# Optimization experiments

Measured on AMD Instinct MI355X. Metric: run time of the kernel, lower is better.

The kernel has to match this reference:

```python
import math
import jax, jax.numpy as jnp
import numpy as np

B, S, D, H = 64, 577, 768, 12
DH = D // H          # 64 per-head dim
FF = 4 * D           # 3072 intermediate
EPS = 1e-6


def layernorm(x, g, b):
    mu = jnp.mean(x, axis=-1, keepdims=True)
    var = jnp.mean(jnp.square(x - mu), axis=-1, keepdims=True)
    return (x - mu) * jax.lax.rsqrt(var + EPS) * g + b


def gelu_tanh(x):
    # NewGELUActivation: 0.5*x*(1+tanh(sqrt(2/pi)*(x+0.044715*x^3)))
    c = math.sqrt(2.0 / math.pi)
    return 0.5 * x * (1.0 + jnp.tanh(c * (x + 0.044715 * x ** 3)))


def setup_inputs() -> dict:
    key = jax.random.key(0)
    ks = jax.random.split(key, 16)
    s_d = 1.0 / math.sqrt(D)
    s_ff = 1.0 / math.sqrt(FF)
    return {
        "x": jax.random.normal(ks[0], (B, S, D), jnp.float32),
        "ln1_g": jnp.ones((D,), jnp.float32),
        "ln1_b": jnp.zeros((D,), jnp.float32),
        # per-head Q/K/V weights stacked: [H, D, DH] (equivalent to H separate Linears)
        "Wq": jax.random.normal(ks[1], (H, D, DH), jnp.float32) * s_d,
        "bq": jax.random.normal(ks[2], (H, DH), jnp.float32) * 0.01,
        "Wk": jax.random.normal(ks[3], (H, D, DH), jnp.float32) * s_d,
        "bk": jax.random.normal(ks[4], (H, DH), jnp.float32) * 0.01,
        "Wv": jax.random.normal(ks[5], (H, D, DH), jnp.float32) * s_d,
        "bv": jax.random.normal(ks[6], (H, DH), jnp.float32) * 0.01,
        "Wo": jax.random.normal(ks[7], (D, D), jnp.float32) * s_d,
        "bo": jax.random.normal(ks[8], (D,), jnp.float32) * 0.01,
        "ln2_g": jnp.ones((D,), jnp.float32),
        "ln2_b": jnp.zeros((D,), jnp.float32),
        "W1": jax.random.normal(ks[9], (D, FF), jnp.float32) * s_d,
        "b1": jax.random.normal(ks[10], (FF,), jnp.float32) * 0.01,
        "W2": jax.random.normal(ks[11], (FF, D), jnp.float32) * s_ff,
        "b2": jax.random.normal(ks[12], (D,), jnp.float32) * 0.01,
    }


def reference(x, ln1_g, ln1_b, Wq, bq, Wk, bk, Wv, bv, Wo, bo,
              ln2_g, ln2_b, W1, b1, W2, b2):
    # --- pre-norm MHA ---
    h = layernorm(x, ln1_g, ln1_b)                       # [B,S,D]
    q = jnp.einsum('bsd,hde->bhse', h, Wq) + bq[:, None, :]
    k = jnp.einsum('bsd,hde->bhse', h, Wk) + bk[:, None, :]
    v = jnp.einsum('bsd,hde->bhse', h, Wv) + bv[:, None, :]
    scores = jnp.einsum('bhse,bhte->bhst', q, k) / math.sqrt(DH)
    probs = jax.nn.softmax(scores, axis=-1)              # [B,H,S,S]
    attn = jnp.einsum('bhst,bhte->bhse', probs, v)       # [B,H,S,DH]
    # concat heads in head order -> [B,S,H*DH]
    concat = attn.transpose(0, 2, 1, 3).reshape(B, S, H * DH)
    x = x + concat @ Wo + bo
    # --- pre-norm MLP ---
    m = layernorm(x, ln2_g, ln2_b)
    m = gelu_tanh(m @ W1 + b1) @ W2 + b2
    return x + m
```

## Files before the change

### kernel.cpp

```cpp
#include <hip/hip_runtime.h>
#include <stdint.h>

constexpr int BZ   = 64;
constexpr int SEQ  = 577;
constexpr int DM   = 768;
constexpr int NH   = 12;
constexpr int HD   = 64;
constexpr int FFD  = 3072;
constexpr int ROWS = BZ * SEQ;
constexpr int BHN  = BZ * NH;
constexpr int VTS  = 640;

typedef __attribute__((ext_vector_type(8))) short bf16x8;
typedef __attribute__((ext_vector_type(4))) float f32x4;

static __device__ __forceinline__ unsigned short f2bf(float f) {
  union { float f; uint32_t u; } v; v.f = f;
  uint32_t r = (v.u + 0x7FFFu + ((v.u >> 16) & 1u)) >> 16;
  return (unsigned short)r;
}

static __device__ __forceinline__ f32x4 mfma16(bf16x8 a, bf16x8 b, f32x4 c) {
  return __builtin_amdgcn_mfma_f32_16x16x32_bf16(a, b, c, 0, 0, 0);
}

static __device__ __forceinline__ void gload_lds16(const unsigned short* g, unsigned short* l) {
  __builtin_amdgcn_global_load_lds((const __attribute__((address_space(1))) unsigned int*)g,
                                   (__attribute__((address_space(3))) unsigned int*)l, 16, 0, 0);
}

__global__ __launch_bounds__(256) void prep_qkv(const float* __restrict__ Wq,
                                                const float* __restrict__ Wk,
                                                const float* __restrict__ Wv,
                                                unsigned short* __restrict__ dst) {
  int tid = blockIdx.x * 256 + threadIdx.x;
  int n = tid / DM, k = tid - n * DM;
  int seg = n / DM;
  int within = n - seg * DM;
  int h = within >> 6, e = within & 63;
  const float* W = (seg == 0) ? Wq : (seg == 1) ? Wk : Wv;
  dst[tid] = f2bf(W[((size_t)h * DM + k) * HD + e]);
}

__global__ __launch_bounds__(256) void prep_t(const float* __restrict__ src,
                                              unsigned short* __restrict__ dst,
                                              int N, int K) {
  int tid = blockIdx.x * 256 + threadIdx.x;
  if (tid >= N * K) return;
  int n = tid / K, k = tid - n * K;
  dst[tid] = f2bf(src[(size_t)k * N + n]);
}

__global__ __launch_bounds__(256) void ln_bf16(const float* __restrict__ X,
                                               const float* __restrict__ g,
                                               const float* __restrict__ b,
                                               unsigned short* __restrict__ out) {
  int row  = blockIdx.x * 4 + (threadIdx.x >> 6);
  int lane = threadIdx.x & 63;
  const float* x = X + (size_t)row * DM;
  float4 v[3];
  float s = 0.f, s2 = 0.f;
#pragma unroll
  for (int i = 0; i < 3; i++) {
    v[i] = *(const float4*)(x + i * 256 + lane * 4);
    s  += v[i].x + v[i].y + v[i].z + v[i].w;
    s2 += v[i].x * v[i].x + v[i].y * v[i].y + v[i].z * v[i].z + v[i].w * v[i].w;
  }
#pragma unroll
  for (int o = 1; o < 64; o <<= 1) { s += __shfl_xor(s, o); s2 += __shfl_xor(s2, o); }
  float mu  = s * (1.f / DM);
  float var = s2 * (1.f / DM) - mu * mu;
  float inv = rsqrtf(var + 1e-6f);
#pragma unroll
  for (int i = 0; i < 3; i++) {
    int c = i * 256 + lane * 4;
    float4 gg = *(const float4*)(g + c);
    float4 bb = *(const float4*)(b + c);
    ushort4 o4;
    o4.x = f2bf((v[i].x - mu) * inv * gg.x + bb.x);
    o4.y = f2bf((v[i].y - mu) * inv * gg.y + bb.y);
    o4.z = f2bf((v[i].z - mu) * inv * gg.z + bb.z);
    o4.w = f2bf((v[i].w - mu) * inv * gg.w + bb.w);
    *(ushort4*)(out + (size_t)row * DM + c) = o4;
  }
}

template <int EPI>
__global__ __launch_bounds__(256) void gemm_bt(
    const unsigned short* __restrict__ A, const unsigned short* __restrict__ Bt,
    int M, int N, int K,
    const float* __restrict__ bias0, const float* __restrict__ bias1,
    const float* __restrict__ bias2, const float* __restrict__ xres,
    float* __restrict__ outf,
    unsigned short* __restrict__ ob0, unsigned short* __restrict__ ob1,
    unsigned short* __restrict__ ob2) {
  __shared__ __align__(16) unsigned short sA[128 * 32];
  __shared__ __align__(16) unsigned short sB[128 * 32];
  const int tid  = threadIdx.x;
  const int wave = tid >> 6, lane = tid & 63;
  const int l15 = lane & 15, quad = lane >> 4;
  const int m0 = blockIdx.y * 128, n0 = blockIdx.x * 128;
  const int wm = (wave >> 1) * 64, wn = (wave & 1) * 64;

  f32x4 acc[4][4] = {};
  const int nkt = K >> 5;
  for (int kt = 0; kt < nkt; ++kt) {
#pragma unroll
    for (int i = 0; i < 2; i++) {
      int c = tid + i * 256;
      int row = c >> 2, kc = (c & 3) << 3;
      int ra = m0 + row; if (ra >= M) ra = M - 1;
      gload_lds16(A  + (size_t)ra * K         + (kt << 5) + kc, sA + row * 32 + kc);
      gload_lds16(Bt + (size_t)(n0 + row) * K + (kt << 5) + kc, sB + row * 32 + kc);
    }
    __syncthreads();
    bf16x8 aF[4], bF[4];
#pragma unroll
    for (int mi = 0; mi < 4; mi++) aF[mi] = *(const bf16x8*)(sA + (wm + mi * 16 + l15) * 32 + quad * 8);
#pragma unroll
    for (int ni = 0; ni < 4; ni++) bF[ni] = *(const bf16x8*)(sB + (wn + ni * 16 + l15) * 32 + quad * 8);
#pragma unroll
    for (int mi = 0; mi < 4; mi++)
#pragma unroll
      for (int ni = 0; ni < 4; ni++) acc[mi][ni] = mfma16(aF[mi], bF[ni], acc[mi][ni]);
    __syncthreads();
  }

#pragma unroll
  for (int mi = 0; mi < 4; mi++) {
#pragma unroll
    for (int r = 0; r < 4; r++) {
      int mg = m0 + wm + mi * 16 + quad * 4 + r;
      if (mg >= M) continue;
      if constexpr (EPI == 0) {
        int bb = mg / SEQ, ss = mg - bb * SEQ;
        int seg = n0 / DM;
        int within0 = n0 - seg * DM + wn;
#pragma unroll
        for (int ni = 0; ni < 4; ni++) {
          int wcol = within0 + ni * 16 + l15;
          int h = wcol >> 6, e = wcol & 63;
          float val = acc[mi][ni][r];
          if (seg == 0) {
            float qv = (val + bias0[wcol]) * 0.125f;
            ob0[((size_t)(bb * NH + h) * SEQ + ss) * HD + e] = f2bf(qv);
          } else if (seg == 1) {
            float kv = val + bias1[wcol];
            ob1[((size_t)(bb * NH + h) * SEQ + ss) * HD + e] = f2bf(kv);
          } else {
            float vv = val + bias2[wcol];
            ob2[((size_t)(bb * NH + h) * HD + e) * VTS + ss] = f2bf(vv);
          }
        }
      } else if constexpr (EPI == 1) {
        size_t base = (size_t)mg * DM;
#pragma unroll
        for (int ni = 0; ni < 4; ni++) {
          int col = n0 + wn + ni * 16 + l15;
          outf[base + col] = xres[base + col] + acc[mi][ni][r] + bias0[col];
        }
      } else if constexpr (EPI == 2) {
        size_t base = (size_t)mg * FFD;
#pragma unroll
        for (int ni = 0; ni < 4; ni++) {
          int col = n0 + wn + ni * 16 + l15;
          float xv = acc[mi][ni][r] + bias0[col];
          float u  = 0.7978845608028654f * (xv + 0.044715f * xv * xv * xv);
          float uc = fminf(fmaxf(u, -15.f), 15.f);
          float t  = __expf(2.f * uc);
          float gel = 0.5f * xv * (1.f + (t - 1.f) / (t + 1.f));
          ob0[base + col] = f2bf(gel);
        }
      } else {
        size_t base = (size_t)mg * DM;
#pragma unroll
        for (int ni = 0; ni < 4; ni++) {
          int col = n0 + wn + ni * 16 + l15;
          outf[base + col] += acc[mi][ni][r] + bias0[col];
        }
      }
    }
  }
}

__global__ __launch_bounds__(256) void attn_fused(
    const unsigned short* __restrict__ Q, const unsigned short* __restrict__ Kb,
    const unsigned short* __restrict__ Vt, unsigned short* __restrict__ Cc) {
  __shared__ __align__(16) unsigned short sK[64 * 72];
  __shared__ __align__(16) unsigned short sV[64 * 72];
  __shared__ __align__(16) unsigned short sP[4][16 * 72];
  const int tid  = threadIdx.x;
  const int wave = tid >> 6, lane = tid & 63;
  const int quad = lane >> 4, l15 = lane & 15;
  const int bh = blockIdx.y;
  const int q0 = blockIdx.x * 64;

  int qr = q0 + wave * 16 + l15; if (qr > SEQ - 1) qr = SEQ - 1;
  const unsigned short* qrow = Q + ((size_t)bh * SEQ + qr) * HD;
  bf16x8 aQ0 = *(const bf16x8*)(qrow + quad * 8);
  bf16x8 aQ1 = *(const bf16x8*)(qrow + 32 + quad * 8);

  float m[4], l[4];
  f32x4 accO[4] = {};
#pragma unroll
  for (int r = 0; r < 4; r++) { m[r] = -3e38f; l[r] = 0.f; }

  for (int t0 = 0; t0 < SEQ; t0 += 64) {
#pragma unroll
    for (int i = 0; i < 2; i++) {
      int c = tid + i * 256;
      int row = c >> 3, col = (c & 7) << 3;
      int tk = t0 + row; if (tk > SEQ - 1) tk = SEQ - 1;
      bf16x8 vk = *(const bf16x8*)(Kb + ((size_t)bh * SEQ + tk) * HD + col);
      bf16x8 vv = *(const bf16x8*)(Vt + ((size_t)bh * HD + row) * VTS + t0 + col);
      *(bf16x8*)(sK + row * 72 + col) = vk;
      *(bf16x8*)(sV + row * 72 + col) = vv;
    }
    __syncthreads();

    f32x4 s4[4];
#pragma unroll
    for (int ni = 0; ni < 4; ni++) {
      bf16x8 b0 = *(const bf16x8*)(sK + (ni * 16 + l15) * 72 + quad * 8);
      bf16x8 b1 = *(const bf16x8*)(sK + (ni * 16 + l15) * 72 + 32 + quad * 8);
      f32x4 a = {0.f, 0.f, 0.f, 0.f};
      a = mfma16(aQ0, b0, a);
      a = mfma16(aQ1, b1, a);
      s4[ni] = a;
    }
#pragma unroll
    for (int ni = 0; ni < 4; ni++) {
      if (t0 + ni * 16 + l15 >= SEQ) {
#pragma unroll
        for (int r = 0; r < 4; r++) s4[ni][r] = -3e38f;
      }
    }
    float mn[4], alpha[4], ts[4];
#pragma unroll
    for (int r = 0; r < 4; r++) {
      float tm = fmaxf(fmaxf(s4[0][r], s4[1][r]), fmaxf(s4[2][r], s4[3][r]));
#pragma unroll
      for (int o = 1; o < 16; o <<= 1) tm = fmaxf(tm, __shfl_xor(tm, o));
      mn[r] = fmaxf(m[r], tm);
      alpha[r] = __expf(m[r] - mn[r]);
      m[r] = mn[r];
      ts[r] = 0.f;
    }
#pragma unroll
    for (int ni = 0; ni < 4; ni++) {
#pragma unroll
      for (int r = 0; r < 4; r++) {
        float p = __expf(s4[ni][r] - mn[r]);
        ts[r] += p;
        sP[wave][(quad * 4 + r) * 72 + ni * 16 + l15] = f2bf(p);
      }
    }
#pragma unroll
    for (int r = 0; r < 4; r++) {
#pragma unroll
      for (int o = 1; o < 16; o <<= 1) ts[r] += __shfl_xor(ts[r], o);
      l[r] = l[r] * alpha[r] + ts[r];
#pragma unroll
      for (int ni = 0; ni < 4; ni++) accO[ni][r] *= alpha[r];
    }
    bf16x8 aP0 = *(const bf16x8*)(sP[wave] + l15 * 72 + quad * 8);
    bf16x8 aP1 = *(const bf16x8*)(sP[wave] + l15 * 72 + 32 + quad * 8);
#pragma unroll
    for (int ni = 0; ni < 4; ni++) {
      bf16x8 v0 = *(const bf16x8*)(sV + (ni * 16 + l15) * 72 + quad * 8);
      bf16x8 v1 = *(const bf16x8*)(sV + (ni * 16 + l15) * 72 + 32 + quad * 8);
      accO[ni] = mfma16(aP0, v0, accO[ni]);
      accO[ni] = mfma16(aP1, v1, accO[ni]);
    }
    __syncthreads();
  }

  int bb = bh / NH, h = bh - bb * NH;
#pragma unroll
  for (int r = 0; r < 4; r++) {
    int ss = q0 + wave * 16 + quad * 4 + r;
    if (ss < SEQ) {
      float inv = 1.f / l[r];
      size_t base = ((size_t)bb * SEQ + ss) * DM + h * HD;
#pragma unroll
      for (int ni = 0; ni < 4; ni++)
        Cc[base + ni * 16 + l15] = f2bf(accO[ni][r] * inv);
    }
  }
}

extern "C" void kernel_launch(void* const* d_in, const int* in_sizes, int n_in,
                              void* d_out, int out_size, void* d_ws, size_t ws_size,
                              hipStream_t stream) {
  (void)in_sizes; (void)n_in; (void)out_size; (void)ws_size;
  const float* x     = (const float*)d_in[0];
  const float* ln1_g = (const float*)d_in[1];
  const float* ln1_b = (const float*)d_in[2];
  const float* Wq    = (const float*)d_in[3];
  const float* bq    = (const float*)d_in[4];
  const float* Wk    = (const float*)d_in[5];
  const float* bk    = (const float*)d_in[6];
  const float* Wv    = (const float*)d_in[7];
  const float* bv    = (const float*)d_in[8];
  const float* Wo    = (const float*)d_in[9];
  const float* bo    = (const float*)d_in[10];
  const float* ln2_g = (const float*)d_in[11];
  const float* ln2_b = (const float*)d_in[12];
  const float* W1    = (const float*)d_in[13];
  const float* b1    = (const float*)d_in[14];
  const float* W2    = (const float*)d_in[15];
  const float* b2    = (const float*)d_in[16];
  float* out = (float*)d_out;

  char* ws = (char*)d_ws;
  size_t off = 0;
  auto alloc = [&](size_t bytes) -> unsigned short* {
    unsigned short* p = (unsigned short*)(ws + off);
    off += (bytes + 255) & ~(size_t)255;
    return p;
  };
  unsigned short* h_bf  = alloc((size_t)ROWS * DM * 2);
  unsigned short* q_bf  = alloc((size_t)BHN * SEQ * HD * 2);
  unsigned short* k_bf  = alloc((size_t)BHN * SEQ * HD * 2);
  unsigned short* vt_bf = alloc((size_t)BHN * HD * VTS * 2);
  unsigned short* cc_bf = alloc((size_t)ROWS * DM * 2);
  unsigned short* g_bf = q_bf;
  unsigned short* wqkv_t = alloc((size_t)2304 * 768 * 2);
  unsigned short* w1_t   = alloc((size_t)3072 * 768 * 2);
  unsigned short* w2_t   = alloc((size_t)768 * 3072 * 2);
  unsigned short* wo_t   = alloc((size_t)768 * 768 * 2);

  prep_qkv<<<(2304 * 768) / 256, 256, 0, stream>>>(Wq, Wk, Wv, wqkv_t);
  prep_t<<<(3072 * 768) / 256, 256, 0, stream>>>(W1, w1_t, 3072, 768);
  prep_t<<<(768 * 3072) / 256, 256, 0, stream>>>(W2, w2_t, 768, 3072);
  prep_t<<<(768 * 768) / 256, 256, 0, stream>>>(Wo, wo_t, 768, 768);

  ln_bf16<<<ROWS / 4, 256, 0, stream>>>(x, ln1_g, ln1_b, h_bf);
  gemm_bt<0><<<dim3(2304 / 128, (ROWS + 127) / 128), 256, 0, stream>>>(
      h_bf, wqkv_t, ROWS, 2304, 768, bq, bk, bv, nullptr, nullptr, q_bf, k_bf, vt_bf);
  attn_fused<<<dim3((SEQ + 63) / 64, BHN), 256, 0, stream>>>(q_bf, k_bf, vt_bf, cc_bf);
  gemm_bt<1><<<dim3(768 / 128, (ROWS + 127) / 128), 256, 0, stream>>>(
      cc_bf, wo_t, ROWS, 768, 768, bo, nullptr, nullptr, x, out, nullptr, nullptr, nullptr);
  ln_bf16<<<ROWS / 4, 256, 0, stream>>>(out, ln2_g, ln2_b, h_bf);
  gemm_bt<2><<<dim3(3072 / 128, (ROWS + 127) / 128), 256, 0, stream>>>(
      h_bf, w1_t, ROWS, 3072, 768, b1, nullptr, nullptr, nullptr, nullptr, g_bf, nullptr, nullptr);
  gemm_bt<3><<<dim3(768 / 128, (ROWS + 127) / 128), 256, 0, stream>>>(
      g_bf, w2_t, ROWS, 768, 3072, b2, nullptr, nullptr, nullptr, out, nullptr, nullptr, nullptr);
}
```

Baseline: 1.599 ms.

## Use 64-wide K tiles with XOR-swizzled LDS and XCD-aware block remap in GEMMs

The GEMM K step goes from 32 to 64, which halves the number of barrier pairs per tile and doubles the MFMA work done between syncs. LDS rows are XOR-swizzled so fragment reads avoid bank conflicts on the wider rows. A 1D grid is remapped so consecutive tiles land on the same XCD (chunks of 8), aiming to improve L2 reuse of A and B tiles. The cost is twice the LDS per block, which may reduce occupancy.

```diff
diff --git a/kernel.cpp b/kernel.cpp
--- a/kernel.cpp
+++ b/kernel.cpp
@@ -88,41 +88,54 @@
 template <int EPI>
 __global__ __launch_bounds__(256) void gemm_bt(
     const unsigned short* __restrict__ A, const unsigned short* __restrict__ Bt,
-    int M, int N, int K,
+    int M, int N, int K, int nbn,
     const float* __restrict__ bias0, const float* __restrict__ bias1,
     const float* __restrict__ bias2, const float* __restrict__ xres,
     float* __restrict__ outf,
     unsigned short* __restrict__ ob0, unsigned short* __restrict__ ob1,
     unsigned short* __restrict__ ob2) {
-  __shared__ __align__(16) unsigned short sA[128 * 32];
-  __shared__ __align__(16) unsigned short sB[128 * 32];
+  __shared__ __align__(16) unsigned short sA[128 * 64];
+  __shared__ __align__(16) unsigned short sB[128 * 64];
   const int tid  = threadIdx.x;
-  const int wave = tid >> 6, lane = tid & 63;
+  const int wave = tid >> 6;
+  const int lane = tid & 63;
   const int l15 = lane & 15, quad = lane >> 4;
-  const int m0 = blockIdx.y * 128, n0 = blockIdx.x * 128;
+
+  const int nb = gridDim.x;
+  const int L = blockIdx.x;
+  const int per = nb >> 3, rem = nb & 7;
+  const int x8 = L & 7, i8 = L >> 3;
+  const int g = x8 * per + (x8 < rem ? x8 : rem) + i8;
+  const int mt = g / nbn, nt = g - mt * nbn;
+  const int m0 = mt * 128, n0 = nt * 128;
   const int wm = (wave >> 1) * 64, wn = (wave & 1) * 64;
 
   f32x4 acc[4][4] = {};
-  const int nkt = K >> 5;
+  const int nkt = K >> 6;
   for (int kt = 0; kt < nkt; ++kt) {
 #pragma unroll
-    for (int i = 0; i < 2; i++) {
-      int c = tid + i * 256;
-      int row = c >> 2, kc = (c & 3) << 3;
+    for (int j = 0; j < 4; j++) {
+      int c = tid + j * 256;
+      int row = c >> 3, col = c & 7;
+      int kc = col ^ (row & 7);
       int ra = m0 + row; if (ra >= M) ra = M - 1;
-      gload_lds16(A  + (size_t)ra * K         + (kt << 5) + kc, sA + row * 32 + kc);
-      gload_lds16(Bt + (size_t)(n0 + row) * K + (kt << 5) + kc, sB + row * 32 + kc);
+      gload_lds16(A  + (size_t)ra * K         + (kt << 6) + kc * 8, sA + c * 8);
+      gload_lds16(Bt + (size_t)(n0 + row) * K + (kt << 6) + kc * 8, sB + c * 8);
     }
     __syncthreads();
-    bf16x8 aF[4], bF[4];
-#pragma unroll
-    for (int mi = 0; mi < 4; mi++) aF[mi] = *(const bf16x8*)(sA + (wm + mi * 16 + l15) * 32 + quad * 8);
-#pragma unroll
-    for (int ni = 0; ni < 4; ni++) bF[ni] = *(const bf16x8*)(sB + (wn + ni * 16 + l15) * 32 + quad * 8);
-#pragma unroll
-    for (int mi = 0; mi < 4; mi++)
-#pragma unroll
-      for (int ni = 0; ni < 4; ni++) acc[mi][ni] = mfma16(aF[mi], bF[ni], acc[mi][ni]);
+#pragma unroll
+    for (int h = 0; h < 2; h++) {
+      bf16x8 aF[4], bF[4];
+      const int swz = ((h << 2) | quad) ^ (l15 & 7);
+#pragma unroll
+      for (int mi = 0; mi < 4; mi++) aF[mi] = *(const bf16x8*)(sA + (wm + mi * 16 + l15) * 64 + swz * 8);
+#pragma unroll
+      for (int ni = 0; ni < 4; ni++) bF[ni] = *(const bf16x8*)(sB + (wn + ni * 16 + l15) * 64 + swz * 8);
+#pragma unroll
+      for (int mi = 0; mi < 4; mi++)
+#pragma unroll
+        for (int ni = 0; ni < 4; ni++) acc[mi][ni] = mfma16(aF[mi], bF[ni], acc[mi][ni]);
+    }
     __syncthreads();
   }
 
@@ -335,15 +348,17 @@
   prep_t<<<(768 * 3072) / 256, 256, 0, stream>>>(W2, w2_t, 768, 3072);
   prep_t<<<(768 * 768) / 256, 256, 0, stream>>>(Wo, wo_t, 768, 768);
 
+  const int MB = (ROWS + 127) / 128;
+
   ln_bf16<<<ROWS / 4, 256, 0, stream>>>(x, ln1_g, ln1_b, h_bf);
-  gemm_bt<0><<<dim3(2304 / 128, (ROWS + 127) / 128), 256, 0, stream>>>(
-      h_bf, wqkv_t, ROWS, 2304, 768, bq, bk, bv, nullptr, nullptr, q_bf, k_bf, vt_bf);
+  gemm_bt<0><<<MB * 18, 256, 0, stream>>>(
+      h_bf, wqkv_t, ROWS, 2304, 768, 18, bq, bk, bv, nullptr, nullptr, q_bf, k_bf, vt_bf);
   attn_fused<<<dim3((SEQ + 63) / 64, BHN), 256, 0, stream>>>(q_bf, k_bf, vt_bf, cc_bf);
-  gemm_bt<1><<<dim3(768 / 128, (ROWS + 127) / 128), 256, 0, stream>>>(
-      cc_bf, wo_t, ROWS, 768, 768, bo, nullptr, nullptr, x, out, nullptr, nullptr, nullptr);
+  gemm_bt<1><<<MB * 6, 256, 0, stream>>>(
+      cc_bf, wo_t, ROWS, 768, 768, 6, bo, nullptr, nullptr, x, out, nullptr, nullptr, nullptr);
   ln_bf16<<<ROWS / 4, 256, 0, stream>>>(out, ln2_g, ln2_b, h_bf);
-  gemm_bt<2><<<dim3(3072 / 128, (ROWS + 127) / 128), 256, 0, stream>>>(
-      h_bf, w1_t, ROWS, 3072, 768, b1, nullptr, nullptr, nullptr, nullptr, g_bf, nullptr, nullptr);
-  gemm_bt<3><<<dim3(768 / 128, (ROWS + 127) / 128), 256, 0, stream>>>(
-      g_bf, w2_t, ROWS, 768, 3072, b2, nullptr, nullptr, nullptr, out, nullptr, nullptr, nullptr);
-}
+  gemm_bt<2><<<MB * 24, 256, 0, stream>>>(
+      h_bf, w1_t, ROWS, 3072, 768, 24, b1, nullptr, nullptr, nullptr, nullptr, g_bf, nullptr, nullptr);
+  gemm_bt<3><<<MB * 6, 256, 0, stream>>>(
+      g_bf, w2_t, ROWS, 768, 3072, 6, b2, nullptr, nullptr, nullptr, out, nullptr, nullptr, nullptr);
+}
```

Measured after the change: 1.475 ms. 7.7% less time.
